# Performance work log

Measured on AMD Instinct MI355X. Metric: run time of the kernel, lower is better.

## Reference

```python
import jax, jax.numpy as jnp
import numpy as np

B, D, F, T, H = 256, 128, 8, 128, 128


def setup_inputs() -> dict:
    key = jax.random.key(0)
    ks = jax.random.split(key, 6)
    inp = jax.random.normal(ks[0], (B, D, F, T), jnp.float32)
    # encode_attn: Linear(F*T + 2*H -> 1); weight laid out as [hidden | cell | x]
    w_attn = jax.random.normal(ks[1], (F * T + 2 * H,), jnp.float32) * 0.02
    b_attn = jax.random.normal(ks[2], (), jnp.float32) * 0.02
    # LSTM (single layer), PyTorch gate order i, f, g, o
    W_ih = jax.random.normal(ks[3], (4 * H, D * F), jnp.float32) * 0.02
    W_hh = jax.random.normal(ks[4], (4 * H, H), jnp.float32) * 0.02
    b_ih = jax.random.normal(ks[5], (4 * H,), jnp.float32) * 0.02
    b_hh = jnp.zeros((4 * H,), jnp.float32)
    return {"input": inp, "w_attn": w_attn, "b_attn": b_attn,
            "W_ih": W_ih, "W_hh": W_hh, "b_ih": b_ih, "b_hh": b_hh}


def reference(input, w_attn, b_attn, W_ih, W_hh, b_ih, b_hh):
    Bd, Dd, Fd, Td = input.shape
    Hd = W_hh.shape[1]
    # split attention weight per cat order: (hidden_state, cell_state, x)
    w_h = w_attn[:Hd]
    w_c = w_attn[Hd:2 * Hd]
    w_x = w_attn[2 * Hd:]
    x_flat = input.reshape(Bd, Dd, Fd * Td)           # [B, D, F*T]
    ex = x_flat @ w_x                                  # [B, D], constant over t
    xs = jnp.moveaxis(input, 3, 0)                     # [T, B, D, F]

    def step(carry, x_t):
        h, c = carry                                   # [B, H] each
        # attention logits: h/c contributions are per-batch scalars broadcast over drives
        e = ex + (h @ w_h + c @ w_c + b_attn)[:, None]  # [B, D]
        a = jax.nn.softmax(e, axis=-1)                 # softmax over drives
        x_hat = (a[:, :, None] * x_t).reshape(Bd, Dd * Fd)  # [B, D*F]
        gates = x_hat @ W_ih.T + h @ W_hh.T + b_ih + b_hh   # [B, 4H]
        i, f, g, o = jnp.split(gates, 4, axis=-1)
        c_new = jax.nn.sigmoid(f) * c + jax.nn.sigmoid(i) * jnp.tanh(g)
        h_new = jax.nn.sigmoid(o) * jnp.tanh(c_new)
        return (h_new, c_new), h_new

    h0 = jnp.zeros((Bd, Hd), input.dtype)
    c0 = jnp.zeros((Bd, Hd), input.dtype)
    _, hs = jax.lax.scan(step, (h0, c0), xs)           # hs: [T, B, H]
    return jnp.transpose(hs, (1, 0, 2))                # [B, T, H] == hidden_states[:, 1:]
```

## Files before the change

### kernel.cpp

```cpp
#include <hip/hip_runtime.h>
#include <cstdint>
#include <cstddef>

#define Bn 256
#define Dn 128
#define Fn 8
#define Tn 128
#define Hn 128
#define Kn 1024
#define Mn 512

typedef float f32x4 __attribute__((ext_vector_type(4)));
typedef short s16x8 __attribute__((ext_vector_type(8)));
typedef _Float16 h16x2 __attribute__((ext_vector_type(2)));
typedef _Float16 h16x8 __attribute__((ext_vector_type(8)));

#if defined(__has_builtin)
#if __has_builtin(__builtin_amdgcn_fdot2)
#define HAVE_FDOT2 1
#else
#define HAVE_FDOT2 0
#endif
#if __has_builtin(__builtin_amdgcn_cvt_pkrtz)
#define HAVE_PKRTZ 1
#else
#define HAVE_PKRTZ 0
#endif
#else
#define HAVE_FDOT2 0
#define HAVE_PKRTZ 0
#endif

__device__ __forceinline__ uint32_t pack2_f16(float a, float b) {
#if HAVE_PKRTZ
  typedef __fp16 fp16x2_t __attribute__((ext_vector_type(2)));
  union { fp16x2_t v; uint32_t u; } cv;
  cv.v = __builtin_amdgcn_cvt_pkrtz(a, b);
  return cv.u;
#else
  union { h16x2 h; uint32_t u; } cv;
  cv.h.x = (_Float16)a; cv.h.y = (_Float16)b;
  return cv.u;
#endif
}
__device__ __forceinline__ float sigm(float x) { return 1.0f / (1.0f + __expf(-x)); }
__device__ __forceinline__ float tanh_fast(float x) { return 1.0f - 2.0f / (__expf(2.0f * x) + 1.0f); }

__global__ __launch_bounds__(256) void k_ex(const float* __restrict__ input,
                                            const float* __restrict__ w_attn,
                                            float* __restrict__ ex) {
  __shared__ float wx[Kn];
  const int tid = threadIdx.x;
  ((float4*)wx)[tid] = ((const float4*)(w_attn + 2 * Hn))[tid];
  __syncthreads();
  const int w = tid >> 6, lane = tid & 63;
  const int gid = blockIdx.x * 4 + w;
  const float4* xp = (const float4*)(input + (size_t)gid * Kn);
  const float4* wx4 = (const float4*)wx;
  float acc = 0.f;
#pragma unroll
  for (int r = 0; r < 4; ++r) {
    float4 x = xp[lane + r * 64];
    float4 ww = wx4[lane + r * 64];
    acc += x.x * ww.x + x.y * ww.y + x.z * ww.z + x.w * ww.w;
  }
#pragma unroll
  for (int off = 32; off; off >>= 1) acc += __shfl_xor(acc, off);
  if (lane == 0) ex[gid] = acc;
}

__global__ __launch_bounds__(256) void k_prep(const float* __restrict__ W_ih,
                                              const float* __restrict__ W_hh,
                                              unsigned short* __restrict__ whf,
                                              uint32_t* __restrict__ whhp) {
  const int bid = blockIdx.x;
  const int tid = threadIdx.x;
  if (bid < 256) {
    const int gid = bid * 256 + tid;
    const int lane = gid & 63;
    const int kt = (gid >> 6) & 31;
    const int mt = gid >> 11;
    const int row = mt * 16 + (lane & 15);
    const int col = kt * 32 + (lane >> 4) * 8;
    const float* src = W_ih + row * Kn + col;
    uint4 ph;
    ph.x = pack2_f16(src[0], src[1]);
    ph.y = pack2_f16(src[2], src[3]);
    ph.z = pack2_f16(src[4], src[5]);
    ph.w = pack2_f16(src[6], src[7]);
    ((uint4*)whf)[gid] = ph;
  } else {
    const int g = (bid - 256) * 256 + tid;
    const int j = g & 511, kk = g >> 9;
    float2 wv = ((const float2*)(W_hh + (size_t)j * Hn))[kk];
    h16x2 t2; t2.x = (_Float16)wv.x; t2.y = (_Float16)wv.y;
    union { h16x2 h; uint32_t u; } cv; cv.h = t2;
    whhp[kk * 512 + j] = cv.u;
  }
}

__global__ __launch_bounds__(256, 2) void k_gates(
    const float* __restrict__ input, const float* __restrict__ ex,
    const unsigned short* __restrict__ whf,
    unsigned short* __restrict__ gx) {
  __shared__ __align__(16) unsigned char smem[34816];
  __shared__ float a_lds[Dn];
  __shared__ float sred[8];
  unsigned short* buf0 = (unsigned short*)smem;
  unsigned short* buf1 = buf0 + 8192;
  _Float16* lds_out = (_Float16*)smem;

  const int tid = threadIdx.x;
  const int bid = blockIdx.x;
  const int p = (bid >> 3) & 3;
  const int b = (bid & 7) | ((bid >> 5) << 3);
  const int w = tid >> 6;
  const int lane = tid & 63;
  const int quad = lane >> 4;
  const int l15 = lane & 15;

  float v = (tid < Dn) ? ex[b * Dn + tid] : -3.4e38f;
  float m = v;
#pragma unroll
  for (int off = 32; off; off >>= 1) m = fmaxf(m, __shfl_xor(m, off));
  if (lane == 0) sred[w] = m;
  __syncthreads();
  m = fmaxf(fmaxf(sred[0], sred[1]), fmaxf(sred[2], sred[3]));
  float e = (tid < Dn) ? __expf(v - m) : 0.f;
  float s = e;
#pragma unroll
  for (int off = 32; off; off >>= 1) s += __shfl_xor(s, off);
  if (lane == 0) sred[4 + w] = s;
  __syncthreads();
  s = sred[4] + sred[5] + sred[6] + sred[7];
  if (tid < Dn) a_lds[tid] = e / s;

  f32x4 acc[2][8];
#pragma unroll
  for (int i = 0; i < 2; ++i)
#pragma unroll
    for (int j = 0; j < 8; ++j) { f32x4 z = {0.f, 0.f, 0.f, 0.f}; acc[i][j] = z; }

  const float* xb = input + (size_t)b * Kn * Tn;
  const int mtg0 = p * 8 + w * 2;

  h16x8 wcur[4], wnxt[4];
#pragma unroll
  for (int mt = 0; mt < 2; ++mt)
#pragma unroll
    for (int kf = 0; kf < 2; ++kf) {
      const size_t fo = (((size_t)(mtg0 + mt) * 32 + kf) * 64 + lane) * 8;
      wcur[mt * 2 + kf] = *(const h16x8*)(whf + fo);
    }

  __syncthreads();

  float xr[2][2][8];
#pragma unroll
  for (int ck = 0; ck < 2; ++ck)
#pragma unroll
    for (int ct = 0; ct < 2; ++ct) {
      const int kb = 2 * w + ck;
      const float* col = xb + (size_t)(kb * 8) * Tn + lane + 64 * ct;
#pragma unroll
      for (int j = 0; j < 8; ++j) xr[ck][ct][j] = col[(size_t)j * Tn];
    }
#pragma unroll
  for (int ck = 0; ck < 2; ++ck) {
    const int kb = 2 * w + ck;
    const float av = a_lds[kb];
#pragma unroll
    for (int ct = 0; ct < 2; ++ct) {
      const int tt = lane + 64 * ct;
      uint4 pk;
      pk.x = pack2_f16(av * xr[ck][ct][0], av * xr[ck][ct][1]);
      pk.y = pack2_f16(av * xr[ck][ct][2], av * xr[ck][ct][3]);
      pk.z = pack2_f16(av * xr[ck][ct][4], av * xr[ck][ct][5]);
      pk.w = pack2_f16(av * xr[ck][ct][6], av * xr[ck][ct][7]);
      *(uint4*)(buf0 + (size_t)(kb * 128 + tt) * 8) = pk;
    }
  }
  __syncthreads();

  for (int kt = 0; kt < 16; ++kt) {
    unsigned short* cur = (kt & 1) ? buf1 : buf0;
    unsigned short* nxt = (kt & 1) ? buf0 : buf1;
    if (kt < 15) {
      const int k0n = (kt + 1) * 64;
#pragma unroll
      for (int ck = 0; ck < 2; ++ck)
#pragma unroll
        for (int ct = 0; ct < 2; ++ct) {
          const int kb = 2 * w + ck;
          const float* col = xb + (size_t)(k0n + kb * 8) * Tn + lane + 64 * ct;
#pragma unroll
          for (int j = 0; j < 8; ++j) xr[ck][ct][j] = col[(size_t)j * Tn];
        }
#pragma unroll
      for (int mt = 0; mt < 2; ++mt)
#pragma unroll
        for (int kf = 0; kf < 2; ++kf) {
          const size_t fo = (((size_t)(mtg0 + mt) * 32 + (kt + 1) * 2 + kf) * 64 + lane) * 8;
          wnxt[mt * 2 + kf] = *(const h16x8*)(whf + fo);
        }
    }
#pragma unroll
    for (int kf = 0; kf < 2; ++kf) {
      h16x8 bfr[8];
      const int kbr = kf * 4 + quad;
#pragma unroll
      for (int nt = 0; nt < 8; ++nt)
        bfr[nt] = *(const h16x8*)(cur + (size_t)(kbr * 128 + nt * 16 + l15) * 8);
#pragma unroll
      for (int mt = 0; mt < 2; ++mt)
#pragma unroll
        for (int nt = 0; nt < 8; ++nt) {
          acc[mt][nt] = __builtin_amdgcn_mfma_f32_16x16x32_f16(wcur[mt * 2 + kf], bfr[nt], acc[mt][nt], 0, 0, 0);
        }
    }
    if (kt < 15) {
#pragma unroll
      for (int ck = 0; ck < 2; ++ck) {
        const int kb = 2 * w + ck;
        const float av = a_lds[(kt + 1) * 8 + kb];
#pragma unroll
        for (int ct = 0; ct < 2; ++ct) {
          const int tt = lane + 64 * ct;
          uint4 pk;
          pk.x = pack2_f16(av * xr[ck][ct][0], av * xr[ck][ct][1]);
          pk.y = pack2_f16(av * xr[ck][ct][2], av * xr[ck][ct][3]);
          pk.z = pack2_f16(av * xr[ck][ct][4], av * xr[ck][ct][5]);
          pk.w = pack2_f16(av * xr[ck][ct][6], av * xr[ck][ct][7]);
          *(uint4*)(nxt + (size_t)(kb * 128 + tt) * 8) = pk;
        }
      }
#pragma unroll
      for (int i = 0; i < 4; ++i) wcur[i] = wnxt[i];
    }
    __syncthreads();
  }

#pragma unroll
  for (int mt = 0; mt < 2; ++mt)
#pragma unroll
    for (int nt = 0; nt < 8; ++nt)
#pragma unroll
      for (int r = 0; r < 4; ++r) {
        const int jl = (w * 2 + mt) * 16 + quad * 4 + r;
        lds_out[jl * 136 + nt * 16 + l15] = (_Float16)acc[mt][nt][r];
      }
  __syncthreads();
  {
    const int jr = tid >> 1, half = tid & 1;
    const uint4* lsrc = (const uint4*)(lds_out + jr * 136 + half * 64);
    uint4* gdst = (uint4*)(gx + ((size_t)(b * Mn + p * 128 + jr)) * Tn + half * 64);
#pragma unroll
    for (int i = 0; i < 8; ++i) gdst[i] = lsrc[i];
  }
}

__global__ __launch_bounds__(256) void k_rec(
    const unsigned short* __restrict__ gx, const uint32_t* __restrict__ whhp,
    const float* __restrict__ b_ih, const float* __restrict__ b_hh,
    float* __restrict__ out) {
  __shared__ unsigned short gxl[512 * 130];
  __shared__ __align__(16) _Float16 h2l[2][Hn];

  const int tid = threadIdx.x;
  const int b = blockIdx.x;

  {
    const uint4* src = (const uint4*)(gx + (size_t)b * Mn * Tn);
#pragma unroll
    for (int it = 0; it < 32; ++it) {
      const int c = it * 256 + tid;
      const int row = c >> 4, off = c & 15;
      uint4 vv = src[c];
      uint32_t* dst = (uint32_t*)((char*)gxl + (size_t)row * 260 + off * 16);
      dst[0] = vv.x; dst[1] = vv.y; dst[2] = vv.z; dst[3] = vv.w;
    }
  }
  const int w = tid >> 6, l = tid & 63;
  const bool lo = (l < 32);
  const int d = w * 32 + (l & 31);
  const int j0 = d + (lo ? 0 : 128);
  const int j1 = j0 + 256;
  const float bs0 = b_ih[j0] + b_hh[j0];
  const float bs1 = b_ih[j1] + b_hh[j1];
  h16x2 wr0[64], wr1[64];
#pragma unroll
  for (int kk = 0; kk < 64; ++kk) {
    union { uint32_t u; h16x2 h; } c0, c1;
    c0.u = whhp[kk * 512 + j0];
    c1.u = whhp[kk * 512 + j1];
    wr0[kk] = c0.h; wr1[kk] = c1.h;
  }
  if (tid < Hn) h2l[0][tid] = (_Float16)0.f;
  float c_st = 0.f;
  __syncthreads();

  float* outp = out + (size_t)b * Tn * Hn;
  for (int t = 0; t < Tn; ++t) {
    float g0 = bs0 + (float)(*(const _Float16*)&gxl[j0 * 130 + t]);
    float g1 = bs1 + (float)(*(const _Float16*)&gxl[j1 * 130 + t]);
    float a0 = 0.f, a1 = 0.f, a2 = 0.f, a3 = 0.f;
    float d0 = 0.f, d1 = 0.f, d2 = 0.f, d3 = 0.f;
    const h16x8* hv = (const h16x8*)(&h2l[t & 1][0]);
#pragma unroll
    for (int q = 0; q < 16; ++q) {
      union { h16x8 v; h16x2 pr[4]; } u; u.v = hv[q];
#if HAVE_FDOT2
      a0 = __builtin_amdgcn_fdot2(wr0[q * 4 + 0], u.pr[0], a0, false);
      a1 = __builtin_amdgcn_fdot2(wr0[q * 4 + 1], u.pr[1], a1, false);
      a2 = __builtin_amdgcn_fdot2(wr0[q * 4 + 2], u.pr[2], a2, false);
      a3 = __builtin_amdgcn_fdot2(wr0[q * 4 + 3], u.pr[3], a3, false);
      d0 = __builtin_amdgcn_fdot2(wr1[q * 4 + 0], u.pr[0], d0, false);
      d1 = __builtin_amdgcn_fdot2(wr1[q * 4 + 1], u.pr[1], d1, false);
      d2 = __builtin_amdgcn_fdot2(wr1[q * 4 + 2], u.pr[2], d2, false);
      d3 = __builtin_amdgcn_fdot2(wr1[q * 4 + 3], u.pr[3], d3, false);
#else
#pragma unroll
      for (int z = 0; z < 4; ++z) {
        a0 += (float)wr0[q * 4 + z].x * (float)u.pr[z].x + (float)wr0[q * 4 + z].y * (float)u.pr[z].y;
        d0 += (float)wr1[q * 4 + z].x * (float)u.pr[z].x + (float)wr1[q * 4 + z].y * (float)u.pr[z].y;
      }
#endif
    }
    const float a = (a0 + a1) + (a2 + a3) + g0;
    const float bb = (d0 + d1) + (d2 + d3) + g1;
    const float aX = __shfl_xor(a, 32);
    const float bX = __shfl_xor(bb, 32);
    const float gi = lo ? a : aX;
    const float gf = lo ? aX : a;
    const float gg = lo ? bb : bX;
    const float go = lo ? bX : bb;
    c_st = sigm(gf) * c_st + sigm(gi) * tanh_fast(gg);
    const float hnew = sigm(go) * tanh_fast(c_st);
    if (lo) {
      outp[t * Hn + d] = hnew;
      h2l[(t + 1) & 1][d] = (_Float16)hnew;
    }
    __syncthreads();
  }
}

extern "C" void kernel_launch(void* const* d_in, const int* in_sizes, int n_in,
                              void* d_out, int out_size, void* d_ws, size_t ws_size,
                              hipStream_t stream) {
  (void)in_sizes; (void)n_in; (void)out_size; (void)ws_size;
  const float* input = (const float*)d_in[0];
  const float* w_attn = (const float*)d_in[1];
  const float* W_ih = (const float*)d_in[3];
  const float* W_hh = (const float*)d_in[4];
  const float* b_ih = (const float*)d_in[5];
  const float* b_hh = (const float*)d_in[6];
  float* out = (float*)d_out;

  char* ws = (char*)d_ws;
  float* ex = (float*)ws;
  unsigned short* whf = (unsigned short*)(ws + 131072);
  uint32_t* whhp = (uint32_t*)(ws + 1179648);
  unsigned short* gxw = (unsigned short*)(ws + 1310720);

  k_ex<<<8192, 256, 0, stream>>>(input, w_attn, ex);
  k_prep<<<384, 256, 0, stream>>>(W_ih, W_hh, whf, whhp);
  k_gates<<<1024, 256, 0, stream>>>(input, ex, whf, gxw);
  k_rec<<<Bn, 256, 0, stream>>>(gxw, whhp, b_ih, b_hh, out);
}
```

Measured before the change: 357.2 us.

## Use MFMA for recurrent h@W_hh matvec in LSTM step kernel

Replaces the per-thread fdot2 recurrent dot products with 16x16x32 f16 MFMA instructions. W_hh is repacked into MFMA B-fragment layout held in registers, and h is broadcast as the A operand. Lanes then pick their gate value from the accumulator tiles. Most of each MFMA tile is wasted because h holds only one row per batch, and all rows of A are identical. The gain would come from lower instruction count on the serial recurrence path.

```diff
diff --git a/kernel.cpp b/kernel.cpp
--- a/kernel.cpp
+++ b/kernel.cpp
@@ -16,18 +16,12 @@
 typedef _Float16 h16x8 __attribute__((ext_vector_type(8)));
 
 #if defined(__has_builtin)
-#if __has_builtin(__builtin_amdgcn_fdot2)
-#define HAVE_FDOT2 1
-#else
-#define HAVE_FDOT2 0
-#endif
 #if __has_builtin(__builtin_amdgcn_cvt_pkrtz)
 #define HAVE_PKRTZ 1
 #else
 #define HAVE_PKRTZ 0
 #endif
 #else
-#define HAVE_FDOT2 0
 #define HAVE_PKRTZ 0
 #endif
 
@@ -72,7 +66,7 @@
 __global__ __launch_bounds__(256) void k_prep(const float* __restrict__ W_ih,
                                               const float* __restrict__ W_hh,
                                               unsigned short* __restrict__ whf,
-                                              uint32_t* __restrict__ whhp) {
+                                              unsigned short* __restrict__ whh) {
   const int bid = blockIdx.x;
   const int tid = threadIdx.x;
   if (bid < 256) {
@@ -91,11 +85,18 @@
     ((uint4*)whf)[gid] = ph;
   } else {
     const int g = (bid - 256) * 256 + tid;
-    const int j = g & 511, kk = g >> 9;
-    float2 wv = ((const float2*)(W_hh + (size_t)j * Hn))[kk];
-    h16x2 t2; t2.x = (_Float16)wv.x; t2.y = (_Float16)wv.y;
-    union { h16x2 h; uint32_t u; } cv; cv.h = t2;
-    whhp[kk * 512 + j] = cv.u;
+    const int l = g & 63;
+    const int kf = (g >> 6) & 3;
+    const int nt = g >> 8;
+    const int row = nt * 16 + (l & 15);
+    const int col = kf * 32 + (l >> 4) * 8;
+    const float* src = W_hh + (size_t)row * Hn + col;
+    uint4 ph;
+    ph.x = pack2_f16(src[0], src[1]);
+    ph.y = pack2_f16(src[2], src[3]);
+    ph.z = pack2_f16(src[4], src[5]);
+    ph.w = pack2_f16(src[6], src[7]);
+    ((uint4*)whh)[g] = ph;
   }
 }
 
@@ -259,8 +260,8 @@
   }
 }
 
-__global__ __launch_bounds__(256) void k_rec(
-    const unsigned short* __restrict__ gx, const uint32_t* __restrict__ whhp,
+__global__ __launch_bounds__(256, 1) void k_rec(
+    const unsigned short* __restrict__ gx, const unsigned short* __restrict__ whh,
     const float* __restrict__ b_ih, const float* __restrict__ b_hh,
     float* __restrict__ out) {
   __shared__ unsigned short gxl[512 * 130];
@@ -287,47 +288,47 @@
   const int j1 = j0 + 256;
   const float bs0 = b_ih[j0] + b_hh[j0];
   const float bs1 = b_ih[j1] + b_hh[j1];
-  h16x2 wr0[64], wr1[64];
-#pragma unroll
-  for (int kk = 0; kk < 64; ++kk) {
-    union { uint32_t u; h16x2 h; } c0, c1;
-    c0.u = whhp[kk * 512 + j0];
-    c1.u = whhp[kk * 512 + j1];
-    wr0[kk] = c0.h; wr1[kk] = c1.h;
+
+  h16x8 wf[8][4];
+#pragma unroll
+  for (int ntl = 0; ntl < 8; ++ntl) {
+    const int nt = (ntl >> 1) * 8 + 2 * w + (ntl & 1);
+#pragma unroll
+    for (int kf = 0; kf < 4; ++kf) {
+      const size_t fo = (((size_t)nt * 4 + kf) * 64 + l) * 8;
+      wf[ntl][kf] = *(const h16x8*)(whh + fo);
+    }
   }
   if (tid < Hn) h2l[0][tid] = (_Float16)0.f;
   float c_st = 0.f;
   __syncthreads();
 
   float* outp = out + (size_t)b * Tn * Hn;
+  const int aoff = (l >> 4) * 8;
   for (int t = 0; t < Tn; ++t) {
-    float g0 = bs0 + (float)(*(const _Float16*)&gxl[j0 * 130 + t]);
-    float g1 = bs1 + (float)(*(const _Float16*)&gxl[j1 * 130 + t]);
-    float a0 = 0.f, a1 = 0.f, a2 = 0.f, a3 = 0.f;
-    float d0 = 0.f, d1 = 0.f, d2 = 0.f, d3 = 0.f;
-    const h16x8* hv = (const h16x8*)(&h2l[t & 1][0]);
-#pragma unroll
-    for (int q = 0; q < 16; ++q) {
-      union { h16x8 v; h16x2 pr[4]; } u; u.v = hv[q];
-#if HAVE_FDOT2
-      a0 = __builtin_amdgcn_fdot2(wr0[q * 4 + 0], u.pr[0], a0, false);
-      a1 = __builtin_amdgcn_fdot2(wr0[q * 4 + 1], u.pr[1], a1, false);
-      a2 = __builtin_amdgcn_fdot2(wr0[q * 4 + 2], u.pr[2], a2, false);
-      a3 = __builtin_amdgcn_fdot2(wr0[q * 4 + 3], u.pr[3], a3, false);
-      d0 = __builtin_amdgcn_fdot2(wr1[q * 4 + 0], u.pr[0], d0, false);
-      d1 = __builtin_amdgcn_fdot2(wr1[q * 4 + 1], u.pr[1], d1, false);
-      d2 = __builtin_amdgcn_fdot2(wr1[q * 4 + 2], u.pr[2], d2, false);
-      d3 = __builtin_amdgcn_fdot2(wr1[q * 4 + 3], u.pr[3], d3, false);
-#else
-#pragma unroll
-      for (int z = 0; z < 4; ++z) {
-        a0 += (float)wr0[q * 4 + z].x * (float)u.pr[z].x + (float)wr0[q * 4 + z].y * (float)u.pr[z].y;
-        d0 += (float)wr1[q * 4 + z].x * (float)u.pr[z].x + (float)wr1[q * 4 + z].y * (float)u.pr[z].y;
-      }
-#endif
-    }
-    const float a = (a0 + a1) + (a2 + a3) + g0;
-    const float bb = (d0 + d1) + (d2 + d3) + g1;
+    const float g0 = bs0 + (float)(*(const _Float16*)&gxl[j0 * 130 + t]);
+    const float g1 = bs1 + (float)(*(const _Float16*)&gxl[j1 * 130 + t]);
+    const _Float16* hb = &h2l[t & 1][0];
+    h16x8 af0 = *(const h16x8*)(hb + 0 * 32 + aoff);
+    h16x8 af1 = *(const h16x8*)(hb + 1 * 32 + aoff);
+    h16x8 af2 = *(const h16x8*)(hb + 2 * 32 + aoff);
+    h16x8 af3 = *(const h16x8*)(hb + 3 * 32 + aoff);
+    f32x4 acc[8];
+#pragma unroll
+    for (int ntl = 0; ntl < 8; ++ntl) {
+      f32x4 z = {0.f, 0.f, 0.f, 0.f};
+      z = __builtin_amdgcn_mfma_f32_16x16x32_f16(af0, wf[ntl][0], z, 0, 0, 0);
+      z = __builtin_amdgcn_mfma_f32_16x16x32_f16(af1, wf[ntl][1], z, 0, 0, 0);
+      z = __builtin_amdgcn_mfma_f32_16x16x32_f16(af2, wf[ntl][2], z, 0, 0, 0);
+      z = __builtin_amdgcn_mfma_f32_16x16x32_f16(af3, wf[ntl][3], z, 0, 0, 0);
+      acc[ntl] = z;
+    }
+    const float va = (l < 16) ? acc[0][0] : (l < 32) ? acc[1][0]
+                   : (l < 48) ? acc[2][0] : acc[3][0];
+    const float vb = (l < 16) ? acc[4][0] : (l < 32) ? acc[5][0]
+                   : (l < 48) ? acc[6][0] : acc[7][0];
+    const float a = va + g0;
+    const float bb = vb + g1;
     const float aX = __shfl_xor(a, 32);
     const float bX = __shfl_xor(bb, 32);
     const float gi = lo ? a : aX;
@@ -359,11 +360,11 @@
   char* ws = (char*)d_ws;
   float* ex = (float*)ws;
   unsigned short* whf = (unsigned short*)(ws + 131072);
-  uint32_t* whhp = (uint32_t*)(ws + 1179648);
+  unsigned short* whh = (unsigned short*)(ws + 1179648);
   unsigned short* gxw = (unsigned short*)(ws + 1310720);
 
   k_ex<<<8192, 256, 0, stream>>>(input, w_attn, ex);
-  k_prep<<<384, 256, 0, stream>>>(W_ih, W_hh, whf, whhp);
+  k_prep<<<288, 256, 0, stream>>>(W_ih, W_hh, whf, whh);
   k_gates<<<1024, 256, 0, stream>>>(input, ex, whf, gxw);
-  k_rec<<<Bn, 256, 0, stream>>>(gxw, whhp, b_ih, b_hh, out);
-}
+  k_rec<<<Bn, 256, 0, stream>>>(gxw, whh, b_ih, b_hh, out);
+}
```

Result: faster. 341.6 us (-4.3%).
